# Kernel tuning notes

Measured on AMD Instinct MI355X. Metric: run time of the kernel, lower is better.

The kernel has to match this reference:

```python
import jax, jax.numpy as jnp
import numpy as np

N_NODES = 50000
N_RAND_EDGES = 800000
K_HEADS = 4
D = 64
EPS = 1e-8


def setup_inputs() -> dict:
    key = jax.random.key(0)
    k1, k2, k3, k4, k5, k6 = jax.random.split(key, 6)
    x = jax.random.normal(k1, (N_NODES, D), dtype=jnp.float32)
    # edge_index without self loops (module removes then re-adds them), then append self loops
    dst = jax.random.randint(k2, (N_RAND_EDGES,), 0, N_NODES)
    off = jax.random.randint(k3, (N_RAND_EDGES,), 1, N_NODES)
    src = (dst + off) % N_NODES  # guaranteed src != dst
    loops = jnp.arange(N_NODES)
    adj = jnp.stack([jnp.concatenate([dst, loops]), jnp.concatenate([src, loops])]).astype(jnp.int64)
    e = jax.random.uniform(k4, (N_NODES, K_HEADS), dtype=jnp.float32)
    stdv = 1.0 / np.sqrt(D)
    weights = jax.random.uniform(k5, (K_HEADS, D, D), minval=-stdv, maxval=stdv, dtype=jnp.float32)
    # xavier_uniform(gain=1.414) on [K, 2D, 1]
    bound = 1.414 * np.sqrt(6.0 / (2 * D + 1))
    a = jax.random.uniform(k6, (K_HEADS, 2 * D, 1), minval=-bound, maxval=bound, dtype=jnp.float32)
    return {"x": x, "adj": adj, "e": e, "weights": weights, "a": a}


def reference(x, adj, e, weights, a):
    N = x.shape[0]
    O = weights.shape[2]
    dst, src = adj[0], adj[1]  # aggregation destination = adj[0], source = adj[1]
    # per-head projection: h[k] = x @ weights[k]  -> [K, N, O]
    h = jnp.einsum('nd,kdo->kno', x, weights)
    # split attention vector: edge_h @ a == <h[dst], a[:O]> + <h[src], a[O:]>
    a_dst = a[:, :O, 0]   # [K, O]
    a_src = a[:, O:, 0]   # [K, O]
    alpha_dst = jnp.einsum('kno,ko->kn', h, a_dst)  # [K, N]
    alpha_src = jnp.einsum('kno,ko->kn', h, a_src)  # [K, N]
    logits = jax.nn.leaky_relu(alpha_dst[:, dst] + alpha_src[:, src], 0.01)  # [K, E]
    # global (per-head) max subtraction, as in the original
    edge_e = jnp.exp(logits - jnp.max(logits, axis=1, keepdims=True))  # [K, E]
    seg = lambda v: jax.ops.segment_sum(v, dst, num_segments=N)
    denom = jax.vmap(seg)(edge_e) + EPS                                 # [K, N]
    num = jax.vmap(seg)(edge_e[:, :, None] * h[:, src])                 # [K, N, O]
    outputs = num / denom[:, :, None]                                   # [K, N, O]
    out = jnp.einsum('nk,kno->no', e, outputs)                          # mixture over K
    return out + x  # residual
```

## Files before the change

kernel.cpp:

```cpp
#include <hip/hip_runtime.h>
#include <hip/hip_bf16.h>

#define KH 4
#define DIM 64
#define EPSV 1e-8f
#define BIN_BLKS 768

typedef __attribute__((ext_vector_type(8))) short bf16x8;
typedef __attribute__((ext_vector_type(4))) float f32x4;
typedef __attribute__((ext_vector_type(2))) float f32x2;

__device__ __forceinline__ float lrelu(float s) { return s > 0.0f ? s : 0.01f * s; }
__device__ __forceinline__ float blo(unsigned u) { return __uint_as_float(u << 16); }
__device__ __forceinline__ float bhi(unsigned u) { return __uint_as_float(u & 0xFFFF0000u); }
__device__ __forceinline__ unsigned short f2b(float f) {
    unsigned u = __float_as_uint(f);
    u += 0x7FFFu + ((u >> 16) & 1u);
    return (unsigned short)(u >> 16);
}

__device__ __forceinline__ unsigned char f2e4m3(float f) {
    unsigned u = __float_as_uint(f);
    unsigned sgn = (u >> 31) << 7;
    float af = fabsf(f);
    if (af >= 0.015625f) {
        unsigned mag = u & 0x7FFFFFFFu;
        unsigned biased = mag - (120u << 23);
        unsigned em = biased >> 20;
        unsigned rem = biased & 0xFFFFFu;
        em += (rem > 0x80000u) ? 1u : ((rem == 0x80000u) ? (em & 1u) : 0u);
        if (em > 126u) em = 126u;
        return (unsigned char)(sgn | em);
    } else {
        int m = (int)rintf(af * 512.0f);
        if (m >= 8) return (unsigned char)(sgn | 8u);
        return (unsigned char)(sgn | (unsigned)m);
    }
}

__device__ __forceinline__ void e4m3x4_to_f32(unsigned v, float& h0, float& h1,
                                              float& h2, float& h3) {
#if __has_builtin(__builtin_amdgcn_cvt_pk_f32_fp8)
    f32x2 lo = __builtin_amdgcn_cvt_pk_f32_fp8(v, false);
    f32x2 hi = __builtin_amdgcn_cvt_pk_f32_fp8(v, true);
    h0 = lo.x; h1 = lo.y; h2 = hi.x; h3 = hi.y;
#else
    auto dec = [](unsigned b) -> float {
        unsigned s = b >> 7, em = b & 0x7Fu;
        float r;
        if (em >= 8u) r = __uint_as_float((em << 20) + (120u << 23));
        else r = (float)em * 0.001953125f;
        return s ? -r : r;
    };
    h0 = dec(v & 0xFF); h1 = dec((v >> 8) & 0xFF);
    h2 = dec((v >> 16) & 0xFF); h3 = dec(v >> 24);
#endif
}

__global__ void __launch_bounds__(256, 4)
k_hidden(const float* __restrict__ x,
         const float* __restrict__ W,
         const float* __restrict__ a,
         unsigned* __restrict__ h8,
         float* __restrict__ adst,
         float* __restrict__ asrc,
         int* __restrict__ cnt, int N) {
    int t = threadIdx.x;
    int gid = blockIdx.x * 256 + t;
    if (gid < N) cnt[gid] = 0;
    int k = t >> 6;
    int l = t & 63;
    int s = l & 15;
    int q = l >> 4;
    int n0 = blockIdx.x * 16;

    const float* Wk = W + k * DIM * DIM;
    bf16x8 Bf[4][2];
#pragma unroll
    for (int tile = 0; tile < 4; ++tile)
#pragma unroll
        for (int c = 0; c < 2; ++c) {
            const float* wp = Wk + (size_t)(32 * c + 8 * q) * DIM + 16 * tile + s;
#pragma unroll
            for (int j = 0; j < 8; ++j)
                Bf[tile][c][j] = (short)f2b(wp[(size_t)j * DIM]);
        }
    float ad[4], as_[4];
#pragma unroll
    for (int tile = 0; tile < 4; ++tile) {
        ad[tile]  = a[k * 2 * DIM + 16 * tile + s];
        as_[tile] = a[k * 2 * DIM + DIM + 16 * tile + s];
    }

    bf16x8 Af[2];
#pragma unroll
    for (int c = 0; c < 2; ++c) {
        const float* xp = x + (size_t)(n0 + s) * DIM + 32 * c + 8 * q;
#pragma unroll
        for (int j = 0; j < 8; ++j) Af[c][j] = (short)f2b(xp[j]);
    }

    f32x4 acc[4];
#pragma unroll
    for (int tile = 0; tile < 4; ++tile) {
        acc[tile] = (f32x4){0.f, 0.f, 0.f, 0.f};
#pragma unroll
        for (int c = 0; c < 2; ++c)
            acc[tile] = __builtin_amdgcn_mfma_f32_16x16x32_bf16(
                Af[c], Bf[tile][c], acc[tile], 0, 0, 0);
    }

#pragma unroll
    for (int r = 0; r < 4; ++r) {
        float vd = 0.f, vs = 0.f;
#pragma unroll
        for (int tile = 0; tile < 4; ++tile) {
            vd = fmaf(acc[tile][r], ad[tile], vd);
            vs = fmaf(acc[tile][r], as_[tile], vs);
        }
#pragma unroll
        for (int off = 1; off < 16; off <<= 1) {
            vd += __shfl_xor(vd, off);
            vs += __shfl_xor(vs, off);
        }
        if (s == 0) {
            int n = n0 + 4 * q + r;
            adst[n * KH + k] = vd;
            asrc[n * KH + k] = vs;
        }
    }

    __shared__ unsigned char hb[16 * DIM * KH];
#pragma unroll
    for (int tile = 0; tile < 4; ++tile)
#pragma unroll
        for (int r = 0; r < 4; ++r) {
            int n = 4 * q + r, o = 16 * tile + s;
            hb[(n * DIM + o) * KH + k] = f2e4m3(acc[tile][r]);
        }
    __syncthreads();
    const unsigned* hb4 = (const unsigned*)hb;
#pragma unroll
    for (int it = 0; it < 4; ++it) {
        int i = it * 256 + t;
        h8[(size_t)n0 * DIM + i] = hb4[i];
    }
}

__global__ void k_bin(const int* __restrict__ dst, const int* __restrict__ src,
                      const float4* __restrict__ adst4, const float4* __restrict__ asrc4,
                      int* __restrict__ cnt, uint4* __restrict__ slots,
                      int cap, int E) {
    int T = gridDim.x * blockDim.x;
    int tid = blockIdx.x * blockDim.x + threadIdx.x;
    int e = tid;
    for (; e + 3 * T < E; e += 4 * T) {
        int e0 = e, e1 = e + T, e2 = e + 2 * T, e3 = e + 3 * T;
        int dn0 = dst[e0], dn1 = dst[e1], dn2 = dst[e2], dn3 = dst[e3];
        int sn0 = src[e0], sn1 = src[e1], sn2 = src[e2], sn3 = src[e3];
        int sl0 = atomicAdd(&cnt[dn0], 1);
        int sl1 = atomicAdd(&cnt[dn1], 1);
        int sl2 = atomicAdd(&cnt[dn2], 1);
        int sl3 = atomicAdd(&cnt[dn3], 1);
        float4 ad0 = adst4[dn0], as0 = asrc4[sn0];
        float4 ad1 = adst4[dn1], as1 = asrc4[sn1];
        float4 ad2 = adst4[dn2], as2 = asrc4[sn2];
        float4 ad3 = adst4[dn3], as3 = asrc4[sn3];
#define EMIT(sl, dn, sn, ad, as)                                              \
        if (sl < cap) {                                                       \
            uint4 sv;                                                         \
            sv.x = (unsigned)sn;                                              \
            sv.y = (unsigned)f2b(__expf(lrelu(ad.x + as.x))) |                \
                   ((unsigned)f2b(__expf(lrelu(ad.y + as.y))) << 16);         \
            sv.z = (unsigned)f2b(__expf(lrelu(ad.z + as.z))) |                \
                   ((unsigned)f2b(__expf(lrelu(ad.w + as.w))) << 16);         \
            sv.w = 0u;                                                        \
            slots[(size_t)dn * cap + sl] = sv;                                \
        }
        EMIT(sl0, dn0, sn0, ad0, as0)
        EMIT(sl1, dn1, sn1, ad1, as1)
        EMIT(sl2, dn2, sn2, ad2, as2)
        EMIT(sl3, dn3, sn3, ad3, as3)
    }
    for (; e < E; e += T) {
        int dn = dst[e], sn = src[e];
        int sl = atomicAdd(&cnt[dn], 1);
        float4 ad = adst4[dn], as = asrc4[sn];
        EMIT(sl, dn, sn, ad, as)
    }
#undef EMIT
}

__global__ void k_aggr(const int* __restrict__ cnt, const uint4* __restrict__ slots,
                       const unsigned* __restrict__ h8,
                       const float* __restrict__ efeat, const float* __restrict__ x,
                       float* __restrict__ out, int cap, int N) {
    int n = blockIdx.x * 4 + (threadIdx.x >> 6);
    if (n >= N) return;
    int o = threadIdx.x & 63;
    int deg = cnt[n]; if (deg > cap) deg = cap;
    const uint4* bs = slots + (size_t)n * cap;
    float v0 = 0.f, v1 = 0.f, v2 = 0.f, v3 = 0.f;
    float d0 = 0.f, d1 = 0.f, d2 = 0.f, d3 = 0.f;
#define ACC(sv, hv)                                                           \
    {                                                                         \
        float h0, h1, h2, h3;                                                 \
        e4m3x4_to_f32(hv, h0, h1, h2, h3);                                    \
        float w;                                                              \
        w = blo(sv.y); v0 = fmaf(w, h0, v0); d0 += w;                         \
        w = bhi(sv.y); v1 = fmaf(w, h1, v1); d1 += w;                         \
        w = blo(sv.z); v2 = fmaf(w, h2, v2); d2 += w;                         \
        w = bhi(sv.z); v3 = fmaf(w, h3, v3); d3 += w;                         \
    }
    int i = 0;
    for (; i + 4 <= deg; i += 4) {
        uint4 s0 = bs[i + 0], s1 = bs[i + 1], s2 = bs[i + 2], s3 = bs[i + 3];
        unsigned a0 = h8[(size_t)s0.x * DIM + o];
        unsigned a1 = h8[(size_t)s1.x * DIM + o];
        unsigned a2 = h8[(size_t)s2.x * DIM + o];
        unsigned a3 = h8[(size_t)s3.x * DIM + o];
        ACC(s0, a0) ACC(s1, a1) ACC(s2, a2) ACC(s3, a3)
    }
    for (; i < deg; ++i) {
        uint4 sv = bs[i];
        unsigned hv = h8[(size_t)sv.x * DIM + o];
        ACC(sv, hv)
    }
#undef ACC
    float4 ef = ((const float4*)efeat)[n];
    float c0 = ef.x / (d0 + EPSV), c1 = ef.y / (d1 + EPSV);
    float c2 = ef.z / (d2 + EPSV), c3 = ef.w / (d3 + EPSV);
    size_t oi = (size_t)n * DIM + o;
    out[oi] = x[oi] + c0 * v0 + c1 * v1 + c2 * v2 + c3 * v3;
}

extern "C" void kernel_launch(void* const* d_in, const int* in_sizes, int n_in,
                              void* d_out, int out_size, void* d_ws, size_t ws_size,
                              hipStream_t stream) {
    const float* x = (const float*)d_in[0];
    const int* adj = (const int*)d_in[1];
    const float* efeat = (const float*)d_in[2];
    const float* W = (const float*)d_in[3];
    const float* a = (const float*)d_in[4];
    float* out = (float*)d_out;

    int N = in_sizes[0] / DIM;
    int E = in_sizes[1] / 2;
    const int* dst = adj;
    const int* src = adj + E;
    int nbhid = (N + 15) / 16;

    unsigned* h8 = (unsigned*)d_ws;
    float* adst = (float*)(h8 + (size_t)N * DIM);
    float* asrc = adst + (size_t)N * KH;
    int* cnt = (int*)(asrc + (size_t)N * KH);
    uint4* slots = (uint4*)(cnt + N);
    size_t used = (size_t)((char*)slots - (char*)d_ws);
    int cap = (int)((ws_size - used) / ((size_t)N * 16));
    if (cap > 64) cap = 64;

    k_hidden<<<nbhid, 256, 0, stream>>>(x, W, a, h8, adst, asrc, cnt, N);

    k_bin<<<BIN_BLKS, 256, 0, stream>>>(dst, src, (const float4*)adst,
                                        (const float4*)asrc, cnt, slots, cap, E);

    k_aggr<<<(N + 3) / 4, 256, 0, stream>>>(cnt, slots, h8, efeat, x, out, cap, N);
}
```

Baseline: 184.3 us.

## Fuse hidden, bin, and aggregate kernels into one cooperative persistent kernel

Merges the three launches (projection with MFMA, edge binning with atomics, per-node aggregation) into a single cooperative kernel with grid-wide syncs between phases. The grid is sized from occupancy and each phase uses grid-stride loops. The goal is to remove launch gaps and inter-kernel tail effects. In exchange it adds grid.sync costs and occupancy-limited parallelism, because launch_bounds(256,4) caps the grid, and the binning unroll drops from 4 to 3.

```diff
diff --git a/kernel.cpp b/kernel.cpp
--- a/kernel.cpp
+++ b/kernel.cpp
@@ -1,10 +1,12 @@
 #include <hip/hip_runtime.h>
 #include <hip/hip_bf16.h>
+#include <hip/hip_cooperative_groups.h>
+
+namespace cg = cooperative_groups;
 
 #define KH 4
 #define DIM 64
 #define EPSV 1e-8f
-#define BIN_BLKS 768
 
 typedef __attribute__((ext_vector_type(8))) short bf16x8;
 typedef __attribute__((ext_vector_type(4))) float f32x4;
@@ -58,180 +60,182 @@
 }
 
 __global__ void __launch_bounds__(256, 4)
-k_hidden(const float* __restrict__ x,
-         const float* __restrict__ W,
-         const float* __restrict__ a,
-         unsigned* __restrict__ h8,
-         float* __restrict__ adst,
-         float* __restrict__ asrc,
-         int* __restrict__ cnt, int N) {
+k_fused(const float* __restrict__ x, const int* __restrict__ adj,
+        const float* __restrict__ efeat, const float* __restrict__ W,
+        const float* __restrict__ a,
+        unsigned* __restrict__ h8, float* __restrict__ adst,
+        float* __restrict__ asrc, int* __restrict__ cnt,
+        uint4* __restrict__ slots, float* __restrict__ out,
+        int cap, int N, int E, int nbhid) {
+    cg::grid_group grid = cg::this_grid();
+    const int* dst = adj;
+    const int* src = adj + E;
     int t = threadIdx.x;
-    int gid = blockIdx.x * 256 + t;
-    if (gid < N) cnt[gid] = 0;
     int k = t >> 6;
     int l = t & 63;
     int s = l & 15;
     int q = l >> 4;
-    int n0 = blockIdx.x * 16;
-
-    const float* Wk = W + k * DIM * DIM;
-    bf16x8 Bf[4][2];
-#pragma unroll
-    for (int tile = 0; tile < 4; ++tile)
-#pragma unroll
-        for (int c = 0; c < 2; ++c) {
-            const float* wp = Wk + (size_t)(32 * c + 8 * q) * DIM + 16 * tile + s;
-#pragma unroll
-            for (int j = 0; j < 8; ++j)
-                Bf[tile][c][j] = (short)f2b(wp[(size_t)j * DIM]);
-        }
-    float ad[4], as_[4];
-#pragma unroll
-    for (int tile = 0; tile < 4; ++tile) {
-        ad[tile]  = a[k * 2 * DIM + 16 * tile + s];
-        as_[tile] = a[k * 2 * DIM + DIM + 16 * tile + s];
-    }
-
-    bf16x8 Af[2];
-#pragma unroll
-    for (int c = 0; c < 2; ++c) {
-        const float* xp = x + (size_t)(n0 + s) * DIM + 32 * c + 8 * q;
-#pragma unroll
-        for (int j = 0; j < 8; ++j) Af[c][j] = (short)f2b(xp[j]);
-    }
-
-    f32x4 acc[4];
-#pragma unroll
-    for (int tile = 0; tile < 4; ++tile) {
-        acc[tile] = (f32x4){0.f, 0.f, 0.f, 0.f};
-#pragma unroll
-        for (int c = 0; c < 2; ++c)
-            acc[tile] = __builtin_amdgcn_mfma_f32_16x16x32_bf16(
-                Af[c], Bf[tile][c], acc[tile], 0, 0, 0);
-    }
-
-#pragma unroll
-    for (int r = 0; r < 4; ++r) {
-        float vd = 0.f, vs = 0.f;
+
+    for (int i = blockIdx.x * 256 + t; i < N; i += gridDim.x * 256) cnt[i] = 0;
+
+    {
+        const float* Wk = W + k * DIM * DIM;
+        bf16x8 Bf[4][2];
+#pragma unroll
+        for (int tile = 0; tile < 4; ++tile)
+#pragma unroll
+            for (int c = 0; c < 2; ++c) {
+                const float* wp = Wk + (size_t)(32 * c + 8 * q) * DIM + 16 * tile + s;
+#pragma unroll
+                for (int j = 0; j < 8; ++j)
+                    Bf[tile][c][j] = (short)f2b(wp[(size_t)j * DIM]);
+            }
+        float ad[4], as_[4];
 #pragma unroll
         for (int tile = 0; tile < 4; ++tile) {
-            vd = fmaf(acc[tile][r], ad[tile], vd);
-            vs = fmaf(acc[tile][r], as_[tile], vs);
-        }
-#pragma unroll
-        for (int off = 1; off < 16; off <<= 1) {
-            vd += __shfl_xor(vd, off);
-            vs += __shfl_xor(vs, off);
-        }
-        if (s == 0) {
-            int n = n0 + 4 * q + r;
-            adst[n * KH + k] = vd;
-            asrc[n * KH + k] = vs;
-        }
-    }
-
-    __shared__ unsigned char hb[16 * DIM * KH];
-#pragma unroll
-    for (int tile = 0; tile < 4; ++tile)
-#pragma unroll
-        for (int r = 0; r < 4; ++r) {
-            int n = 4 * q + r, o = 16 * tile + s;
-            hb[(n * DIM + o) * KH + k] = f2e4m3(acc[tile][r]);
-        }
-    __syncthreads();
-    const unsigned* hb4 = (const unsigned*)hb;
-#pragma unroll
-    for (int it = 0; it < 4; ++it) {
-        int i = it * 256 + t;
-        h8[(size_t)n0 * DIM + i] = hb4[i];
-    }
-}
-
-__global__ void k_bin(const int* __restrict__ dst, const int* __restrict__ src,
-                      const float4* __restrict__ adst4, const float4* __restrict__ asrc4,
-                      int* __restrict__ cnt, uint4* __restrict__ slots,
-                      int cap, int E) {
-    int T = gridDim.x * blockDim.x;
-    int tid = blockIdx.x * blockDim.x + threadIdx.x;
-    int e = tid;
-    for (; e + 3 * T < E; e += 4 * T) {
-        int e0 = e, e1 = e + T, e2 = e + 2 * T, e3 = e + 3 * T;
-        int dn0 = dst[e0], dn1 = dst[e1], dn2 = dst[e2], dn3 = dst[e3];
-        int sn0 = src[e0], sn1 = src[e1], sn2 = src[e2], sn3 = src[e3];
-        int sl0 = atomicAdd(&cnt[dn0], 1);
-        int sl1 = atomicAdd(&cnt[dn1], 1);
-        int sl2 = atomicAdd(&cnt[dn2], 1);
-        int sl3 = atomicAdd(&cnt[dn3], 1);
-        float4 ad0 = adst4[dn0], as0 = asrc4[sn0];
-        float4 ad1 = adst4[dn1], as1 = asrc4[sn1];
-        float4 ad2 = adst4[dn2], as2 = asrc4[sn2];
-        float4 ad3 = adst4[dn3], as3 = asrc4[sn3];
+            ad[tile]  = a[k * 2 * DIM + 16 * tile + s];
+            as_[tile] = a[k * 2 * DIM + DIM + 16 * tile + s];
+        }
+        __shared__ unsigned char hb[16 * DIM * KH];
+        for (int tile_i = blockIdx.x; tile_i < nbhid; tile_i += gridDim.x) {
+            int n0 = tile_i * 16;
+            __syncthreads();
+            bf16x8 Af[2];
+#pragma unroll
+            for (int c = 0; c < 2; ++c) {
+                const float* xp = x + (size_t)(n0 + s) * DIM + 32 * c + 8 * q;
+#pragma unroll
+                for (int j = 0; j < 8; ++j) Af[c][j] = (short)f2b(xp[j]);
+            }
+            f32x4 acc[4];
+#pragma unroll
+            for (int tile = 0; tile < 4; ++tile) {
+                acc[tile] = (f32x4){0.f, 0.f, 0.f, 0.f};
+#pragma unroll
+                for (int c = 0; c < 2; ++c)
+                    acc[tile] = __builtin_amdgcn_mfma_f32_16x16x32_bf16(
+                        Af[c], Bf[tile][c], acc[tile], 0, 0, 0);
+            }
+#pragma unroll
+            for (int r = 0; r < 4; ++r) {
+                float vd = 0.f, vs = 0.f;
+#pragma unroll
+                for (int tile = 0; tile < 4; ++tile) {
+                    vd = fmaf(acc[tile][r], ad[tile], vd);
+                    vs = fmaf(acc[tile][r], as_[tile], vs);
+                }
+#pragma unroll
+                for (int off = 1; off < 16; off <<= 1) {
+                    vd += __shfl_xor(vd, off);
+                    vs += __shfl_xor(vs, off);
+                }
+                if (s == 0) {
+                    int n = n0 + 4 * q + r;
+                    adst[n * KH + k] = vd;
+                    asrc[n * KH + k] = vs;
+                }
+            }
+#pragma unroll
+            for (int tile = 0; tile < 4; ++tile)
+#pragma unroll
+                for (int r = 0; r < 4; ++r) {
+                    int n = 4 * q + r, o = 16 * tile + s;
+                    hb[(n * DIM + o) * KH + k] = f2e4m3(acc[tile][r]);
+                }
+            __syncthreads();
+            const unsigned* hb4 = (const unsigned*)hb;
+#pragma unroll
+            for (int it = 0; it < 4; ++it) {
+                int i = it * 256 + t;
+                h8[(size_t)n0 * DIM + i] = hb4[i];
+            }
+        }
+    }
+    grid.sync();
+
+    {
+        const float4* adst4 = (const float4*)adst;
+        const float4* asrc4 = (const float4*)asrc;
+        int T = gridDim.x * 256;
+        int e = blockIdx.x * 256 + t;
+        for (; e + 2 * T < E; e += 3 * T) {
+            int e0 = e, e1 = e + T, e2 = e + 2 * T;
+            int dn0 = dst[e0], dn1 = dst[e1], dn2 = dst[e2];
+            int sn0 = src[e0], sn1 = src[e1], sn2 = src[e2];
+            int sl0 = atomicAdd(&cnt[dn0], 1);
+            int sl1 = atomicAdd(&cnt[dn1], 1);
+            int sl2 = atomicAdd(&cnt[dn2], 1);
+            float4 ad0 = adst4[dn0], as0 = asrc4[sn0];
+            float4 ad1 = adst4[dn1], as1 = asrc4[sn1];
+            float4 ad2 = adst4[dn2], as2 = asrc4[sn2];
 #define EMIT(sl, dn, sn, ad, as)                                              \
-        if (sl < cap) {                                                       \
-            uint4 sv;                                                         \
-            sv.x = (unsigned)sn;                                              \
-            sv.y = (unsigned)f2b(__expf(lrelu(ad.x + as.x))) |                \
-                   ((unsigned)f2b(__expf(lrelu(ad.y + as.y))) << 16);         \
-            sv.z = (unsigned)f2b(__expf(lrelu(ad.z + as.z))) |                \
-                   ((unsigned)f2b(__expf(lrelu(ad.w + as.w))) << 16);         \
-            sv.w = 0u;                                                        \
-            slots[(size_t)dn * cap + sl] = sv;                                \
-        }
-        EMIT(sl0, dn0, sn0, ad0, as0)
-        EMIT(sl1, dn1, sn1, ad1, as1)
-        EMIT(sl2, dn2, sn2, ad2, as2)
-        EMIT(sl3, dn3, sn3, ad3, as3)
-    }
-    for (; e < E; e += T) {
-        int dn = dst[e], sn = src[e];
-        int sl = atomicAdd(&cnt[dn], 1);
-        float4 ad = adst4[dn], as = asrc4[sn];
-        EMIT(sl, dn, sn, ad, as)
-    }
+            if (sl < cap) {                                                   \
+                uint4 sv;                                                     \
+                sv.x = (unsigned)sn;                                          \
+                sv.y = (unsigned)f2b(__expf(lrelu(ad.x + as.x))) |            \
+                       ((unsigned)f2b(__expf(lrelu(ad.y + as.y))) << 16);     \
+                sv.z = (unsigned)f2b(__expf(lrelu(ad.z + as.z))) |            \
+                       ((unsigned)f2b(__expf(lrelu(ad.w + as.w))) << 16);     \
+                sv.w = 0u;                                                    \
+                slots[(size_t)dn * cap + sl] = sv;                            \
+            }
+            EMIT(sl0, dn0, sn0, ad0, as0)
+            EMIT(sl1, dn1, sn1, ad1, as1)
+            EMIT(sl2, dn2, sn2, ad2, as2)
+        }
+        for (; e < E; e += T) {
+            int dn = dst[e], sn = src[e];
+            int sl = atomicAdd(&cnt[dn], 1);
+            float4 ad = adst4[dn], as = asrc4[sn];
+            EMIT(sl, dn, sn, ad, as)
+        }
 #undef EMIT
-}
-
-__global__ void k_aggr(const int* __restrict__ cnt, const uint4* __restrict__ slots,
-                       const unsigned* __restrict__ h8,
-                       const float* __restrict__ efeat, const float* __restrict__ x,
-                       float* __restrict__ out, int cap, int N) {
-    int n = blockIdx.x * 4 + (threadIdx.x >> 6);
-    if (n >= N) return;
-    int o = threadIdx.x & 63;
-    int deg = cnt[n]; if (deg > cap) deg = cap;
-    const uint4* bs = slots + (size_t)n * cap;
-    float v0 = 0.f, v1 = 0.f, v2 = 0.f, v3 = 0.f;
-    float d0 = 0.f, d1 = 0.f, d2 = 0.f, d3 = 0.f;
+    }
+    grid.sync();
+
+    {
+        int ngrp = (N + 3) / 4;
+        for (int grp = blockIdx.x; grp < ngrp; grp += gridDim.x) {
+            int n = grp * 4 + k;
+            if (n >= N) continue;
+            int o = l;
+            int deg = cnt[n]; if (deg > cap) deg = cap;
+            const uint4* bs = slots + (size_t)n * cap;
+            float v0 = 0.f, v1 = 0.f, v2 = 0.f, v3 = 0.f;
+            float d0 = 0.f, d1 = 0.f, d2 = 0.f, d3 = 0.f;
 #define ACC(sv, hv)                                                           \
-    {                                                                         \
-        float h0, h1, h2, h3;                                                 \
-        e4m3x4_to_f32(hv, h0, h1, h2, h3);                                    \
-        float w;                                                              \
-        w = blo(sv.y); v0 = fmaf(w, h0, v0); d0 += w;                         \
-        w = bhi(sv.y); v1 = fmaf(w, h1, v1); d1 += w;                         \
-        w = blo(sv.z); v2 = fmaf(w, h2, v2); d2 += w;                         \
-        w = bhi(sv.z); v3 = fmaf(w, h3, v3); d3 += w;                         \
-    }
-    int i = 0;
-    for (; i + 4 <= deg; i += 4) {
-        uint4 s0 = bs[i + 0], s1 = bs[i + 1], s2 = bs[i + 2], s3 = bs[i + 3];
-        unsigned a0 = h8[(size_t)s0.x * DIM + o];
-        unsigned a1 = h8[(size_t)s1.x * DIM + o];
-        unsigned a2 = h8[(size_t)s2.x * DIM + o];
-        unsigned a3 = h8[(size_t)s3.x * DIM + o];
-        ACC(s0, a0) ACC(s1, a1) ACC(s2, a2) ACC(s3, a3)
-    }
-    for (; i < deg; ++i) {
-        uint4 sv = bs[i];
-        unsigned hv = h8[(size_t)sv.x * DIM + o];
-        ACC(sv, hv)
-    }
+            {                                                                 \
+                float h0, h1, h2, h3;                                         \
+                e4m3x4_to_f32(hv, h0, h1, h2, h3);                            \
+                float w;                                                      \
+                w = blo(sv.y); v0 = fmaf(w, h0, v0); d0 += w;                 \
+                w = bhi(sv.y); v1 = fmaf(w, h1, v1); d1 += w;                 \
+                w = blo(sv.z); v2 = fmaf(w, h2, v2); d2 += w;                 \
+                w = bhi(sv.z); v3 = fmaf(w, h3, v3); d3 += w;                 \
+            }
+            int i = 0;
+            for (; i + 4 <= deg; i += 4) {
+                uint4 s0 = bs[i + 0], s1 = bs[i + 1];
+                uint4 s2 = bs[i + 2], s3 = bs[i + 3];
+                unsigned a0 = h8[(size_t)s0.x * DIM + o];
+                unsigned a1 = h8[(size_t)s1.x * DIM + o];
+                unsigned a2 = h8[(size_t)s2.x * DIM + o];
+                unsigned a3 = h8[(size_t)s3.x * DIM + o];
+                ACC(s0, a0) ACC(s1, a1) ACC(s2, a2) ACC(s3, a3)
+            }
+            for (; i < deg; ++i) {
+                uint4 sv = bs[i];
+                unsigned hv = h8[(size_t)sv.x * DIM + o];
+                ACC(sv, hv)
+            }
 #undef ACC
-    float4 ef = ((const float4*)efeat)[n];
-    float c0 = ef.x / (d0 + EPSV), c1 = ef.y / (d1 + EPSV);
-    float c2 = ef.z / (d2 + EPSV), c3 = ef.w / (d3 + EPSV);
-    size_t oi = (size_t)n * DIM + o;
-    out[oi] = x[oi] + c0 * v0 + c1 * v1 + c2 * v2 + c3 * v3;
+            float4 ef = ((const float4*)efeat)[n];
+            float c0 = ef.x / (d0 + EPSV), c1 = ef.y / (d1 + EPSV);
+            float c2 = ef.z / (d2 + EPSV), c3 = ef.w / (d3 + EPSV);
+            size_t oi = (size_t)n * DIM + o;
+            out[oi] = x[oi] + c0 * v0 + c1 * v1 + c2 * v2 + c3 * v3;
+        }
+    }
 }
 
 extern "C" void kernel_launch(void* const* d_in, const int* in_sizes, int n_in,
@@ -246,8 +250,6 @@
 
     int N = in_sizes[0] / DIM;
     int E = in_sizes[1] / 2;
-    const int* dst = adj;
-    const int* src = adj + E;
     int nbhid = (N + 15) / 16;
 
     unsigned* h8 = (unsigned*)d_ws;
@@ -259,10 +261,20 @@
     int cap = (int)((ws_size - used) / ((size_t)N * 16));
     if (cap > 64) cap = 64;
 
-    k_hidden<<<nbhid, 256, 0, stream>>>(x, W, a, h8, adst, asrc, cnt, N);
-
-    k_bin<<<BIN_BLKS, 256, 0, stream>>>(dst, src, (const float4*)adst,
-                                        (const float4*)asrc, cnt, slots, cap, E);
-
-    k_aggr<<<(N + 3) / 4, 256, 0, stream>>>(cnt, slots, h8, efeat, x, out, cap, N);
-}
+    int dev = 0;
+    hipGetDevice(&dev);
+    int numCU = 256;
+    hipDeviceGetAttribute(&numCU, hipDeviceAttributeMultiprocessorCount, dev);
+    int nb = 0;
+    hipOccupancyMaxActiveBlocksPerMultiprocessor(&nb, k_fused, 256, 0);
+    if (nb < 1) nb = 1;
+    int grid = numCU * nb;
+    if (grid > 2048) grid = 2048;
+
+    void* kargs[] = {(void*)&x, (void*)&adj, (void*)&efeat, (void*)&W, (void*)&a,
+                     (void*)&h8, (void*)&adst, (void*)&asrc, (void*)&cnt,
+                     (void*)&slots, (void*)&out,
+                     (void*)&cap, (void*)&N, (void*)&E, (void*)&nbhid};
+    hipLaunchCooperativeKernel((void*)k_fused, dim3(grid), dim3(256),
+                               kargs, 0, stream);
+}
```

Result: slower. 389.6 us (+111.4%).
